# Performance work log

Hardware: AMD Instinct MI355X
Metric: run time of the kernel (lower is better)

The kernel has to match this reference:

```python
import jax, jax.numpy as jnp
import numpy as np

VOCAB, EMBED, HIDDEN, OUT = 32000, 512, 1024, 32000
BATCH, SEQ = 8, 256


def setup_inputs() -> dict:
    key = jax.random.key(0)
    ks = jax.random.split(key, 8)
    s_e = 1.0 / np.sqrt(EMBED)
    s_h = 1.0 / np.sqrt(HIDDEN)
    return {
        "inputs": jax.random.randint(ks[0], (BATCH, SEQ), 0, VOCAB, dtype=jnp.int64),
        "embed_table": jax.random.normal(ks[1], (VOCAB, EMBED), dtype=jnp.float32),
        "W_ih": jax.random.uniform(ks[2], (HIDDEN, EMBED), jnp.float32, -s_h, s_h),
        "W_hh": jax.random.uniform(ks[3], (HIDDEN, HIDDEN), jnp.float32, -s_h, s_h),
        "b_ih": jax.random.uniform(ks[4], (HIDDEN,), jnp.float32, -s_h, s_h),
        "b_hh": jax.random.uniform(ks[5], (HIDDEN,), jnp.float32, -s_h, s_h),
        "W_fc": jax.random.uniform(ks[6], (OUT, HIDDEN), jnp.float32, -s_h, s_h),
        "b_fc": jax.random.uniform(ks[7], (OUT,), jnp.float32, -s_h, s_h),
    }


def reference(inputs, embed_table, W_ih, W_hh, b_ih, b_hh, W_fc, b_fc):
    # embeds: [B, T, E] -> [T, B, E] for scan over time
    embeds = embed_table[inputs]
    x_t = jnp.transpose(embeds, (1, 0, 2))
    # precompute input contribution for all steps: [T, B, H]
    xproj = jnp.einsum("tbe,he->tbh", x_t, W_ih) + b_ih

    def step(h, xp):
        h_new = jnp.tanh(xp + h @ W_hh.T + b_hh)
        return h_new, h_new

    h0 = jnp.zeros((inputs.shape[0], W_hh.shape[0]), dtype=embeds.dtype)
    _, hs = jax.lax.scan(step, h0, xproj)  # hs: [T, B, H]
    # fc projection per step: [T, B, OUT] -> [B, T, OUT]
    logits = jnp.einsum("tbh,oh->tbo", hs, W_fc) + b_fc
    return jnp.transpose(logits, (1, 0, 2))
```

## Files before the change

### kernel.cpp

```cpp
#include <hip/hip_runtime.h>
#include <stdint.h>

#define T_SEQ 256
#define NB    8
#define EMB   512
#define HID   1024
#define NOUT  32000
#define RING  16
#define SEN   0x40004000u

typedef float    f32x4  __attribute__((ext_vector_type(4)));
typedef unsigned int u32x4 __attribute__((ext_vector_type(4)));
typedef __bf16   bf16x8 __attribute__((ext_vector_type(8)));

#define AS1 __attribute__((address_space(1)))
#define AS3 __attribute__((address_space(3)))

__device__ __forceinline__ uint32_t f2bf(float f) {
    uint32_t u = __builtin_bit_cast(uint32_t, f);
    u += 0x7FFFu + ((u >> 16) & 1u);
    return (u >> 16);
}

__device__ __forceinline__ bf16x8 mk_hi(u32x4 a, u32x4 b) {
    u32x4 r;
    r.x = __builtin_amdgcn_perm(a.y, a.x, 0x07060302u);
    r.y = __builtin_amdgcn_perm(a.w, a.z, 0x07060302u);
    r.z = __builtin_amdgcn_perm(b.y, b.x, 0x07060302u);
    r.w = __builtin_amdgcn_perm(b.w, b.z, 0x07060302u);
    return __builtin_bit_cast(bf16x8, r);
}
__device__ __forceinline__ bf16x8 mk_lo(u32x4 a, u32x4 b) {
    u32x4 r;
    r.x = __builtin_amdgcn_perm(a.y, a.x, 0x05040100u);
    r.y = __builtin_amdgcn_perm(a.w, a.z, 0x05040100u);
    r.z = __builtin_amdgcn_perm(b.y, b.x, 0x05040100u);
    r.w = __builtin_amdgcn_perm(b.w, b.z, 0x05040100u);
    return __builtin_bit_cast(bf16x8, r);
}

__global__ __launch_bounds__(256) void k_prologue(
        const int* __restrict__ inputs, const float* __restrict__ embed,
        const float* __restrict__ W_ih, const float* __restrict__ b_ih,
        float* __restrict__ xproj,
        unsigned int* __restrict__ hpk,
        const float* __restrict__ W_fc, unsigned short* __restrict__ wfcb) {
    const int blk = blockIdx.x;
    const int tid = threadIdx.x;

    if (blk < 128) {
        int i = blk * 256 + tid;
        unsigned int* a = hpk + (size_t)i * 4;
#pragma unroll
        for (int j = 0; j < 4; ++j)
            (void)__hip_atomic_exchange(a + j, SEN, __ATOMIC_RELAXED, __HIP_MEMORY_SCOPE_AGENT);
        return;
    }

    if (blk < 640) {
        __shared__ float As[64][33];
        __shared__ float Bs[64][33];
        __shared__ int   idx_s[64];
        const int idx = blk - 128;
        const int bm = idx >> 4, bn = idx & 15;
        if (tid < 64) {
            int m = bm * 64 + tid;
            idx_s[tid] = inputs[(m & 7) * T_SEQ + (m >> 3)];
        }
        __syncthreads();
        const int ty = tid >> 4, tx = tid & 15;
        const int lr = tid >> 2, lc = (tid & 3) * 8;
        float acc[4][4] = {};
        for (int kk = 0; kk < EMB; kk += 32) {
            __syncthreads();
            const float* arow = embed + (size_t)idx_s[lr] * EMB + kk + lc;
            f32x4 a0 = *(const f32x4*)arow;
            f32x4 a1 = *(const f32x4*)(arow + 4);
            const float* brow = W_ih + (size_t)(bn * 64 + lr) * EMB + kk + lc;
            f32x4 b0 = *(const f32x4*)brow;
            f32x4 b1 = *(const f32x4*)(brow + 4);
#pragma unroll
            for (int u = 0; u < 4; ++u) {
                As[lr][lc + u] = a0[u]; As[lr][lc + 4 + u] = a1[u];
                Bs[lr][lc + u] = b0[u]; Bs[lr][lc + 4 + u] = b1[u];
            }
            __syncthreads();
#pragma unroll
            for (int k = 0; k < 32; ++k) {
                float av[4], bv[4];
#pragma unroll
                for (int i = 0; i < 4; ++i) av[i] = As[ty * 4 + i][k];
#pragma unroll
                for (int j = 0; j < 4; ++j) bv[j] = Bs[tx * 4 + j][k];
#pragma unroll
                for (int i = 0; i < 4; ++i)
#pragma unroll
                    for (int j = 0; j < 4; ++j) acc[i][j] += av[i] * bv[j];
            }
        }
#pragma unroll
        for (int i = 0; i < 4; ++i) {
            int m = bm * 64 + ty * 4 + i;
#pragma unroll
            for (int j = 0; j < 4; ++j) {
                int n = bn * 64 + tx * 4 + j;
                xproj[(size_t)m * HID + n] = acc[i][j] + b_ih[n];
            }
        }
        return;
    }

    {
        int i = (blk - 640) * 256 + tid;
        const f32x4* s4 = (const f32x4*)W_fc;
        int n4 = NOUT * HID / 4;
        int stride = 1408 * 256;
        for (int idx2 = i; idx2 < n4; idx2 += stride) {
            f32x4 v = s4[idx2];
            uint2 o;
            o.x = f2bf(v.x) | (f2bf(v.y) << 16);
            o.y = f2bf(v.z) | (f2bf(v.w) << 16);
            ((uint2*)wfcb)[idx2] = o;
        }
    }
}

#define DO_CHUNK(qa, qb, WH, WL, ACC) do {                                      \
    bf16x8 ah = mk_hi(qa, qb);                                                  \
    bf16x8 al = mk_lo(qa, qb);                                                  \
    ACC = __builtin_amdgcn_mfma_f32_16x16x32_bf16(ah, WH, ACC, 0, 0, 0);        \
    ACC = __builtin_amdgcn_mfma_f32_16x16x32_bf16(al, WH, ACC, 0, 0, 0);        \
    ACC = __builtin_amdgcn_mfma_f32_16x16x32_bf16(ah, WL, ACC, 0, 0, 0);        \
} while (0)

__global__ __launch_bounds__(256, 1) void k_rnn(
        const float* __restrict__ W_hh, const float* __restrict__ b_hh,
        const float* __restrict__ xproj,
        unsigned int* __restrict__ hpk ,
        unsigned short* __restrict__ hs ) {
    __shared__ __align__(16) unsigned int hlds[1024];
    __shared__ float part[2][4][16];
    const int tid = threadIdx.x;
    const int w   = tid >> 6;
    const int ln  = tid & 63;
    const int blk = blockIdx.x;
    const int chain  = blk >> 5;
    const int member = blk & 31;
    const int cg = w & 1;
    const int kh = w >> 1;
    const int col0 = member * 32 + cg * 16;
    unsigned int* ring = hpk + (size_t)chain * (RING * 1024);

    const float* wrow = W_hh + (size_t)(col0 + (ln & 15)) * HID;
    bf16x8 whi[16], wlo[16];
#pragma unroll
    for (int cc = 0; cc < 16; ++cc) {
        int k0 = kh * 512 + cc * 32 + (ln >> 4) * 8;
        f32x4 wa = *(const f32x4*)(wrow + k0);
        f32x4 wb = *(const f32x4*)(wrow + k0 + 4);
        float wv[8] = { wa.x, wa.y, wa.z, wa.w, wb.x, wb.y, wb.z, wb.w };
        uint32_t hu[8], lu[8];
#pragma unroll
        for (int j = 0; j < 8; ++j) {
            hu[j] = f2bf(wv[j]);
            float hif = __builtin_bit_cast(float, hu[j] << 16);
            lu[j] = f2bf(wv[j] - hif);
        }
        u32x4 ph = { hu[0] | (hu[1] << 16), hu[2] | (hu[3] << 16),
                     hu[4] | (hu[5] << 16), hu[6] | (hu[7] << 16) };
        u32x4 pl = { lu[0] | (lu[1] << 16), lu[2] | (lu[3] << 16),
                     lu[4] | (lu[5] << 16), lu[6] | (lu[7] << 16) };
        whi[cc] = __builtin_bit_cast(bf16x8, ph);
        wlo[cc] = __builtin_bit_cast(bf16x8, pl);
    }
    const float bhh = (ln < 16) ? b_hh[col0 + ln] : 0.f;

    for (int t = 0; t < T_SEQ; ++t) {
        float xp = 0.f;
        if (kh == 0 && ln < 16)
            xp = xproj[(size_t)(t * NB + chain) * HID + col0 + ln];

        if (t > 0) {
            const unsigned int* hp = ring + (size_t)((t - 1) & (RING - 1)) * 1024
                                          + w * 256 + ln * 4;
            u32x4 q;
            do {
                asm volatile("global_load_dwordx4 %0, %1, off sc0 sc1\n\t"
                             "s_waitcnt vmcnt(0)"
                             : "=&v"(q) : "v"(hp) : "memory");
            } while (q.x == SEN || q.y == SEN || q.z == SEN || q.w == SEN);
            *(u32x4*)&hlds[w * 256 + ln * 4] = q;
        }
        __syncthreads();

        f32x4 acc0 = {0.f, 0.f, 0.f, 0.f}, acc1 = {0.f, 0.f, 0.f, 0.f};
        if (t > 0) {
            const int lsub = (ln >> 4) * 8;
#pragma unroll
            for (int cc = 0; cc < 16; ++cc) {
                int ab = kh * 512 + cc * 32 + lsub;
                u32x4 qa = *(const u32x4*)&hlds[ab];
                u32x4 qb = *(const u32x4*)&hlds[ab + 4];
                if (cc & 1) { DO_CHUNK(qa, qb, whi[cc], wlo[cc], acc1); }
                else        { DO_CHUNK(qa, qb, whi[cc], wlo[cc], acc0); }
            }
        }
        if (ln < 16) part[t & 1][w][ln] = acc0.x + acc1.x;
        __syncthreads();

        if (kh == 0 && ln < 16) {
            float sum = part[t & 1][w][ln] + part[t & 1][w + 2][ln];
            int colp = col0 + ln;
            float x = xp + sum + bhh;
            float h = tanhf(x);
            uint32_t hi = f2bf(h);
            float hif = __builtin_bit_cast(float, hi << 16);
            uint32_t lo = f2bf(h - hif);
            uint32_t pk = (hi << 16) | lo;
            (void)__hip_atomic_exchange(ring + (size_t)(t & (RING - 1)) * 1024 + colp,
                                        pk, __ATOMIC_RELAXED, __HIP_MEMORY_SCOPE_AGENT);
            (void)__hip_atomic_exchange(ring + (size_t)((t + RING - 3) & (RING - 1)) * 1024 + colp,
                                        SEN, __ATOMIC_RELAXED, __HIP_MEMORY_SCOPE_AGENT);
            hs[(size_t)(t * NB + chain) * HID + colp] = (unsigned short)hi;
        }
    }
}

__global__ void k_fc(const unsigned short* __restrict__ A,
                     const unsigned short* __restrict__ Bw,
                     const float* __restrict__ bias,
                     float* __restrict__ out) {
    __shared__ __align__(16) unsigned short As[128 * 32];
    __shared__ __align__(16) unsigned short Bs[128 * 32];
    const int tid = threadIdx.x;
    const int w = tid >> 6, ln = tid & 63;
    const int bm = blockIdx.x, bn = blockIdx.y;
    const int wm = (w >> 1) * 64, wn = (w & 1) * 64;
    const int srow = tid >> 2;
    const int scol = (tid & 3) * 8;
    const unsigned short* Ag = A  + (size_t)(bm * 128 + srow) * 1024 + scol;
    const unsigned short* Bg = Bw + (size_t)(bn * 128 + srow) * 1024 + scol;
    unsigned short* ldsA0 = As + w * 512;
    unsigned short* ldsA1 = As + 2048 + w * 512;
    unsigned short* ldsB0 = Bs + w * 512;
    unsigned short* ldsB1 = Bs + 2048 + w * 512;

    f32x4 acc[4][4] = {};
    const int fr = ln & 15;
    const int kq = (ln >> 4) * 8;

    for (int kk = 0; kk < 1024; kk += 32) {
        __syncthreads();
        __builtin_amdgcn_global_load_lds((const AS1 void*)(Ag + kk),             (AS3 void*)ldsA0, 16, 0, 0);
        __builtin_amdgcn_global_load_lds((const AS1 void*)(Ag + 64 * 1024 + kk), (AS3 void*)ldsA1, 16, 0, 0);
        __builtin_amdgcn_global_load_lds((const AS1 void*)(Bg + kk),             (AS3 void*)ldsB0, 16, 0, 0);
        __builtin_amdgcn_global_load_lds((const AS1 void*)(Bg + 64 * 1024 + kk), (AS3 void*)ldsB1, 16, 0, 0);
        __syncthreads();
        bf16x8 af[4], bf[4];
#pragma unroll
        for (int i = 0; i < 4; ++i)
            af[i] = *(const bf16x8*)&As[(wm + i * 16 + fr) * 32 + kq];
#pragma unroll
        for (int j = 0; j < 4; ++j)
            bf[j] = *(const bf16x8*)&Bs[(wn + j * 16 + fr) * 32 + kq];
#pragma unroll
        for (int i = 0; i < 4; ++i)
#pragma unroll
            for (int j = 0; j < 4; ++j)
                acc[i][j] = __builtin_amdgcn_mfma_f32_16x16x32_bf16(af[i], bf[j], acc[i][j], 0, 0, 0);
    }

    const int fq = ln >> 4;
#pragma unroll
    for (int i = 0; i < 4; ++i) {
#pragma unroll
        for (int j = 0; j < 4; ++j) {
            int n = bn * 128 + wn + j * 16 + fr;
            float bv = bias[n];
#pragma unroll
            for (int r = 0; r < 4; ++r) {
                int m = bm * 128 + wm + i * 16 + fq * 4 + r;
                int t = m >> 3, b = m & 7;
                out[(size_t)b * T_SEQ * NOUT + (size_t)t * NOUT + n] = acc[i][j][r] + bv;
            }
        }
    }
}

extern "C" void kernel_launch(void* const* d_in, const int* in_sizes, int n_in,
                              void* d_out, int out_size, void* d_ws, size_t ws_size,
                              hipStream_t stream) {
    const int*   inputs = (const int*)d_in[0];
    const float* embed  = (const float*)d_in[1];
    const float* W_ih   = (const float*)d_in[2];
    const float* W_hh   = (const float*)d_in[3];
    const float* b_ih   = (const float*)d_in[4];
    const float* b_hh   = (const float*)d_in[5];
    const float* W_fc   = (const float*)d_in[6];
    const float* b_fc   = (const float*)d_in[7];
    float* out = (float*)d_out;

    char* ws = (char*)d_ws;
    unsigned int*   hpk   = (unsigned int*)(ws);
    float*          xproj = (float*)(ws + 524288);
    unsigned short* hs    = (unsigned short*)(ws + 524288 + 8388608);
    unsigned short* wfcb  = (unsigned short*)(ws + 524288 + 8388608 + 4194304);

    k_prologue<<<2048, 256, 0, stream>>>(inputs, embed, W_ih, b_ih, xproj,
                                         hpk, W_fc, wfcb);
    k_rnn<<<256, 256, 0, stream>>>(W_hh, b_hh, xproj, hpk, hs);
    k_fc<<<dim3(16, 250), 256, 0, stream>>>(hs, wfcb, b_fc, out);
}
```

Measured before the change: 773.0 us.

## Split recurrent K across four waves so each wave reads only its own h slice

```diff
diff --git a/kernel.cpp b/kernel.cpp
--- a/kernel.cpp
+++ b/kernel.cpp
@@ -139,45 +139,48 @@
         unsigned int* __restrict__ hpk ,
         unsigned short* __restrict__ hs ) {
     __shared__ __align__(16) unsigned int hlds[1024];
-    __shared__ float part[2][4][16];
+    __shared__ float part[2][4][32];
     const int tid = threadIdx.x;
     const int w   = tid >> 6;
     const int ln  = tid & 63;
     const int blk = blockIdx.x;
     const int chain  = blk >> 5;
     const int member = blk & 31;
-    const int cg = w & 1;
-    const int kh = w >> 1;
-    const int col0 = member * 32 + cg * 16;
+    const int col0 = member * 32;
     unsigned int* ring = hpk + (size_t)chain * (RING * 1024);
 
-    const float* wrow = W_hh + (size_t)(col0 + (ln & 15)) * HID;
-    bf16x8 whi[16], wlo[16];
-#pragma unroll
-    for (int cc = 0; cc < 16; ++cc) {
-        int k0 = kh * 512 + cc * 32 + (ln >> 4) * 8;
-        f32x4 wa = *(const f32x4*)(wrow + k0);
-        f32x4 wb = *(const f32x4*)(wrow + k0 + 4);
-        float wv[8] = { wa.x, wa.y, wa.z, wa.w, wb.x, wb.y, wb.z, wb.w };
-        uint32_t hu[8], lu[8];
-#pragma unroll
-        for (int j = 0; j < 8; ++j) {
-            hu[j] = f2bf(wv[j]);
-            float hif = __builtin_bit_cast(float, hu[j] << 16);
-            lu[j] = f2bf(wv[j] - hif);
-        }
-        u32x4 ph = { hu[0] | (hu[1] << 16), hu[2] | (hu[3] << 16),
-                     hu[4] | (hu[5] << 16), hu[6] | (hu[7] << 16) };
-        u32x4 pl = { lu[0] | (lu[1] << 16), lu[2] | (lu[3] << 16),
-                     lu[4] | (lu[5] << 16), lu[6] | (lu[7] << 16) };
-        whi[cc] = __builtin_bit_cast(bf16x8, ph);
-        wlo[cc] = __builtin_bit_cast(bf16x8, pl);
-    }
-    const float bhh = (ln < 16) ? b_hh[col0 + ln] : 0.f;
+    const float* wrowA = W_hh + (size_t)(col0 + (ln & 15)) * HID;
+    const float* wrowB = W_hh + (size_t)(col0 + 16 + (ln & 15)) * HID;
+    bf16x8 whiA[8], wloA[8], whiB[8], wloB[8];
+#pragma unroll
+    for (int cc = 0; cc < 8; ++cc) {
+        int k0 = w * 256 + cc * 32 + (ln >> 4) * 8;
+#pragma unroll
+        for (int g = 0; g < 2; ++g) {
+            const float* wr = g ? wrowB : wrowA;
+            f32x4 wa = *(const f32x4*)(wr + k0);
+            f32x4 wb = *(const f32x4*)(wr + k0 + 4);
+            float wv[8] = { wa.x, wa.y, wa.z, wa.w, wb.x, wb.y, wb.z, wb.w };
+            uint32_t hu[8], lu[8];
+#pragma unroll
+            for (int j = 0; j < 8; ++j) {
+                hu[j] = f2bf(wv[j]);
+                float hif = __builtin_bit_cast(float, hu[j] << 16);
+                lu[j] = f2bf(wv[j] - hif);
+            }
+            u32x4 ph = { hu[0] | (hu[1] << 16), hu[2] | (hu[3] << 16),
+                         hu[4] | (hu[5] << 16), hu[6] | (hu[7] << 16) };
+            u32x4 pl = { lu[0] | (lu[1] << 16), lu[2] | (lu[3] << 16),
+                         lu[4] | (lu[5] << 16), lu[6] | (lu[7] << 16) };
+            if (g) { whiB[cc] = __builtin_bit_cast(bf16x8, ph); wloB[cc] = __builtin_bit_cast(bf16x8, pl); }
+            else   { whiA[cc] = __builtin_bit_cast(bf16x8, ph); wloA[cc] = __builtin_bit_cast(bf16x8, pl); }
+        }
+    }
+    const float bhh = (w == 0 && ln < 32) ? b_hh[col0 + ln] : 0.f;
 
     for (int t = 0; t < T_SEQ; ++t) {
         float xp = 0.f;
-        if (kh == 0 && ln < 16)
+        if (w == 0 && ln < 32)
             xp = xproj[(size_t)(t * NB + chain) * HID + col0 + ln];
 
         if (t > 0) {
@@ -190,26 +193,37 @@
                              : "=&v"(q) : "v"(hp) : "memory");
             } while (q.x == SEN || q.y == SEN || q.z == SEN || q.w == SEN);
             *(u32x4*)&hlds[w * 256 + ln * 4] = q;
-        }
-        __syncthreads();
-
-        f32x4 acc0 = {0.f, 0.f, 0.f, 0.f}, acc1 = {0.f, 0.f, 0.f, 0.f};
+            asm volatile("s_waitcnt lgkmcnt(0)" ::: "memory");
+            __builtin_amdgcn_sched_barrier(0);
+        }
+
+        f32x4 aA0 = {0.f,0.f,0.f,0.f}, aA1 = {0.f,0.f,0.f,0.f};
+        f32x4 aB0 = {0.f,0.f,0.f,0.f}, aB1 = {0.f,0.f,0.f,0.f};
         if (t > 0) {
             const int lsub = (ln >> 4) * 8;
 #pragma unroll
-            for (int cc = 0; cc < 16; ++cc) {
-                int ab = kh * 512 + cc * 32 + lsub;
+            for (int cc = 0; cc < 8; ++cc) {
+                int ab = w * 256 + cc * 32 + lsub;
                 u32x4 qa = *(const u32x4*)&hlds[ab];
                 u32x4 qb = *(const u32x4*)&hlds[ab + 4];
-                if (cc & 1) { DO_CHUNK(qa, qb, whi[cc], wlo[cc], acc1); }
-                else        { DO_CHUNK(qa, qb, whi[cc], wlo[cc], acc0); }
-            }
-        }
-        if (ln < 16) part[t & 1][w][ln] = acc0.x + acc1.x;
+                if (cc & 1) {
+                    DO_CHUNK(qa, qb, whiA[cc], wloA[cc], aA1);
+                    DO_CHUNK(qa, qb, whiB[cc], wloB[cc], aB1);
+                } else {
+                    DO_CHUNK(qa, qb, whiA[cc], wloA[cc], aA0);
+                    DO_CHUNK(qa, qb, whiB[cc], wloB[cc], aB0);
+                }
+            }
+        }
+        if (ln < 16) {
+            part[t & 1][w][ln]      = aA0.x + aA1.x;
+            part[t & 1][w][16 + ln] = aB0.x + aB1.x;
+        }
         __syncthreads();
 
-        if (kh == 0 && ln < 16) {
-            float sum = part[t & 1][w][ln] + part[t & 1][w + 2][ln];
+        if (w == 0 && ln < 32) {
+            float sum = part[t & 1][0][ln] + part[t & 1][1][ln]
+                      + part[t & 1][2][ln] + part[t & 1][3][ln];
             int colp = col0 + ln;
             float x = xp + sum + bhh;
             float h = tanhf(x);
```

Result: faster. 674.0 us (-12.8%).
